# Performance work log

Measured on AMD Instinct MI355X. Metric: run time of the kernel, lower is better.

Reference implementation:

```python
import jax, jax.numpy as jnp
import numpy as np

B, F, V, D = 16384, 16, 300000, 10


def setup_inputs() -> dict:
    key = jax.random.key(0)
    k1, k2, k3 = jax.random.split(key, 3)
    x = jax.random.randint(k1, (B, F), 0, V)
    emb = jax.random.normal(k2, (F, V, D), dtype=jnp.float32) * 0.01
    lin = jax.random.normal(k3, (V, 1), dtype=jnp.float32) * 0.01
    return {"x": x, "emb": emb, "lin": lin}


def reference(x, emb, lin):
    # x: [B, F] int ids; emb: [F, V, D] per-field embedding tables; lin: [V, 1]
    F_, V_, D_ = emb.shape
    Bsz = x.shape[0]
    # pair indices (i < j), same order as the nested python loops (i outer, j inner)
    ii, jj = jnp.triu_indices(F_, k=1)  # each [P], P = F*(F-1)/2
    # a[p, b] = emb[j_p][ x[b, i_p] ]  (table j indexed by field-i id)
    a = emb[jj[:, None], x[:, ii].T]   # [P, B, D]
    # b[p, b] = emb[i_p][ x[b, j_p] ]
    b = emb[ii[:, None], x[:, jj].T]   # [P, B, D]
    pair = (a * b).transpose(1, 0, 2).reshape(Bsz, -1)  # [B, P*D]
    # self embeddings: emb[i][ x[:, i] ] for each field i, concatenated
    self_e = emb[jnp.arange(F_)[None, :], x].reshape(Bsz, -1)  # [B, F*D]
    # linear term: lin[x].view(-1, F)
    lin_e = lin[x][..., 0]  # [B, F]
    return jnp.concatenate([pair, self_e, lin_e], axis=1)  # [B, P*D + F*D + F]
```

## Files before the change

### kernel.cpp

```cpp
#include <hip/hip_runtime.h>

#define Bsz   16384
#define Fn    16
#define Vn    300000
#define Dn    10
#define OUT_ROW 1376
#define ROWS_PER_BLOCK 4

typedef float f32x2 __attribute__((ext_vector_type(2)));

__device__ const unsigned char PAIR_IJ[120] = {
    1,2,3,4,5,6,7,8,9,10,11,12,13,14,15,
    18,19,20,21,22,23,24,25,26,27,28,29,30,31,
    35,36,37,38,39,40,41,42,43,44,45,46,47,
    52,53,54,55,56,57,58,59,60,61,62,63,
    69,70,71,72,73,74,75,76,77,78,79,
    86,87,88,89,90,91,92,93,94,95,
    103,104,105,106,107,108,109,110,111,
    120,121,122,123,124,125,126,127,
    137,138,139,140,141,142,143,
    154,155,156,157,158,159,
    171,172,173,174,175,
    188,189,190,191,
    205,206,207,
    222,223,
    239
};

__global__ __launch_bounds__(256, 6) void ffm_kernel(
    const int*   __restrict__ x,
    const float* __restrict__ emb,
    const float* __restrict__ lin,
    float*       __restrict__ out)
{
    const int wave = threadIdx.x >> 6;
    const int lane = threadIdx.x & 63;
    const int row  = blockIdx.x * ROWS_PER_BLOCK + wave;

    const int xv = x[row * Fn + (lane & 15)];
    float* orow = out + (size_t)row * OUT_ROW;
    const float lv = lin[xv];

    const int k0t = 1280 + 2 * lane;
    const int pt  = k0t / 10;
    const int d0t = k0t - pt * 10;
    const int ft  = pt - 120;
    const int fts = (ft < 16) ? ft : 0;
    const int xft = __shfl(xv, fts);
    float2 tailv = make_float2(0.f, 0.f);
    if (lane < 40) {
        tailv = *(const float2*)(emb + (unsigned)(fts * Vn + xft) * 10u + d0t);
    }

    float2 A[10], Bv[10];
    bool   pr[10];
    #pragma unroll
    for (int it = 0; it < 10; ++it) {
        const int k0 = 2 * lane + (it << 7);
        const int p  = k0 / 10;
        const int d0 = k0 - p * 10;
        const bool isPair = p < 120;
        pr[it] = isPair;
        const int ij = PAIR_IJ[isPair ? p : 0];
        const int f  = p - 120;
        const int i  = isPair ? (ij >> 4) : f;
        const int j  = isPair ? (ij & 15) : f;
        const int xi = __shfl(xv, i);
        const int xj = __shfl(xv, j);
        A[it]  = *(const float2*)(emb + (unsigned)(j * Vn + xi) * 10u + d0);
        Bv[it] = *(const float2*)(emb + (unsigned)(i * Vn + xj) * 10u + d0);
    }
    #pragma unroll
    for (int it = 0; it < 10; ++it) {
        const int k0 = 2 * lane + (it << 7);
        f32x2 r;
        r.x = pr[it] ? A[it].x * Bv[it].x : A[it].x;
        r.y = pr[it] ? A[it].y * Bv[it].y : A[it].y;
        __builtin_nontemporal_store(r, (f32x2*)(orow + k0));
    }

    if (lane < 40) {
        f32x2 tv; tv.x = tailv.x; tv.y = tailv.y;
        __builtin_nontemporal_store(tv, (f32x2*)(orow + k0t));
    }
    if (lane >= 16 && lane < 32) {
        __builtin_nontemporal_store(lv, orow + 1344 + lane);
    }
}

extern "C" void kernel_launch(void* const* d_in, const int* in_sizes, int n_in,
                              void* d_out, int out_size, void* d_ws, size_t ws_size,
                              hipStream_t stream) {
    const int*   x   = (const int*)d_in[0];
    const float* emb = (const float*)d_in[1];
    const float* lin = (const float*)d_in[2];
    float*       out = (float*)d_out;

    const int blocks = Bsz / ROWS_PER_BLOCK;
    ffm_kernel<<<blocks, 256, 0, stream>>>(x, emb, lin, out);
}
```

Before: 341.0 us.

## Gather B operand directly into LDS via global_load_lds to cut VGPR pressure

Moves the second gathered embedding operand (B) from register float2 loads to per-dword global_load_lds transfers into a per-wave shared buffer. The A operand stays in registers, a block barrier waits for the LDS writes, and the product is formed by reading B back from LDS. The pair table lookup is changed to a wave shuffle and the division by 10 to a multiply-shift. Launch bounds rise to 8 blocks per CU, trading fewer VGPRs for more dword-granular loads, 20KB of LDS per block and an added barrier.

Measured after the change: 340.7 us. About the same (-0.1%).

```diff
diff --git a/kernel.cpp b/kernel.cpp
--- a/kernel.cpp
+++ b/kernel.cpp
@@ -27,12 +27,20 @@
     239
 };
 
-__global__ __launch_bounds__(256, 6) void ffm_kernel(
+__device__ __forceinline__ void gload_lds4(const float* g, void* l) {
+    __builtin_amdgcn_global_load_lds(
+        (const __attribute__((address_space(1))) void*)g,
+        (__attribute__((address_space(3))) void*)l, 4, 0, 0);
+}
+
+__global__ __launch_bounds__(256, 8) void ffm_kernel(
     const int*   __restrict__ x,
     const float* __restrict__ emb,
     const float* __restrict__ lin,
     float*       __restrict__ out)
 {
+    __shared__ float smemB[ROWS_PER_BLOCK][1280];
+
     const int wave = threadIdx.x >> 6;
     const int lane = threadIdx.x & 63;
     const int row  = blockIdx.x * ROWS_PER_BLOCK + wave;
@@ -40,6 +48,43 @@
     const int xv = x[row * Fn + (lane & 15)];
     float* orow = out + (size_t)row * OUT_ROW;
     const float lv = lin[xv];
+
+    const int ijlo = PAIR_IJ[lane];
+    const int ijhi = PAIR_IJ[lane < 56 ? 64 + lane : 0];
+
+    #pragma unroll
+    for (int it = 0; it < 19; ++it) {
+        const int k = lane + (it << 6);
+        const unsigned p = ((unsigned)k * 52429u) >> 19;
+        const int d  = k - 10 * (int)p;
+        const int ij = (p < 64) ? __shfl(ijlo, (int)p) : __shfl(ijhi, (int)p - 64);
+        const bool isPair = p < 120;
+        const int f  = (int)p - 120;
+        const int i  = isPair ? (ij >> 4) : f;
+        const int j  = isPair ? (ij & 15) : f;
+        const int xj = __shfl(xv, j);
+        if (k < 1200) {
+            gload_lds4(emb + (unsigned)(i * Vn + xj) * 10u + d,
+                       (void*)&smemB[wave][it << 6]);
+        }
+    }
+
+    float2 A[10];
+    bool   prm[10];
+    #pragma unroll
+    for (int it = 0; it < 10; ++it) {
+        const int k0 = 2 * lane + (it << 7);
+        const unsigned p = ((unsigned)k0 * 52429u) >> 19;
+        const int d0 = k0 - 10 * (int)p;
+        const bool isPair = p < 120;
+        prm[it] = isPair;
+        const int ij = (p < 64) ? __shfl(ijlo, (int)p) : __shfl(ijhi, (int)p - 64);
+        const int f  = (int)p - 120;
+        const int i  = isPair ? (ij >> 4) : f;
+        const int j  = isPair ? (ij & 15) : f;
+        const int xi = __shfl(xv, i);
+        A[it] = *(const float2*)(emb + (unsigned)(j * Vn + xi) * 10u + d0);
+    }
 
     const int k0t = 1280 + 2 * lane;
     const int pt  = k0t / 10;
@@ -52,30 +97,15 @@
         tailv = *(const float2*)(emb + (unsigned)(fts * Vn + xft) * 10u + d0t);
     }
 
-    float2 A[10], Bv[10];
-    bool   pr[10];
+    __syncthreads();
+
     #pragma unroll
     for (int it = 0; it < 10; ++it) {
         const int k0 = 2 * lane + (it << 7);
-        const int p  = k0 / 10;
-        const int d0 = k0 - p * 10;
-        const bool isPair = p < 120;
-        pr[it] = isPair;
-        const int ij = PAIR_IJ[isPair ? p : 0];
-        const int f  = p - 120;
-        const int i  = isPair ? (ij >> 4) : f;
-        const int j  = isPair ? (ij & 15) : f;
-        const int xi = __shfl(xv, i);
-        const int xj = __shfl(xv, j);
-        A[it]  = *(const float2*)(emb + (unsigned)(j * Vn + xi) * 10u + d0);
-        Bv[it] = *(const float2*)(emb + (unsigned)(i * Vn + xj) * 10u + d0);
-    }
-    #pragma unroll
-    for (int it = 0; it < 10; ++it) {
-        const int k0 = 2 * lane + (it << 7);
+        const float2 b = *(const float2*)&smemB[wave][(it << 7) + 2 * lane];
         f32x2 r;
-        r.x = pr[it] ? A[it].x * Bv[it].x : A[it].x;
-        r.y = pr[it] ? A[it].y * Bv[it].y : A[it].y;
+        r.x = prm[it] ? A[it].x * b.x : A[it].x;
+        r.y = prm[it] ? A[it].y * b.y : A[it].y;
         __builtin_nontemporal_store(r, (f32x2*)(orow + k0));
     }
 
```
